# Performance work log

Hardware: AMD Instinct MI355X
Metric: run time of the kernel (lower is better)

## Reference

```python
import jax, jax.numpy as jnp
import numpy as np

B, L, D, T, S, K = 16, 4095, 768, 768, 64, 8
H = T // 2  # per-direction GRU hidden


def setup_inputs() -> dict:
    key = jax.random.key(0)
    ks = jax.random.split(key, 16)
    sc = 0.05
    hidden = jax.random.normal(ks[0], (B, L, D), jnp.float32)
    attn_len = jax.random.randint(ks[1], (B,), L // 2, L).astype(jnp.int32)
    span_start = jax.random.randint(ks[2], (B, S), 0, L - 16).astype(jnp.int32)
    span_len = jax.random.randint(ks[3], (B, S), 1, 9).astype(jnp.int32)
    return dict(
        hidden=hidden,
        W_ih_f=jax.random.normal(ks[4], (3 * H, D)) * sc,
        W_hh_f=jax.random.normal(ks[5], (3 * H, H)) * sc,
        b_ih_f=jax.random.normal(ks[6], (3 * H,)) * sc,
        b_hh_f=jax.random.normal(ks[7], (3 * H,)) * sc,
        W_ih_b=jax.random.normal(ks[8], (3 * H, D)) * sc,
        W_hh_b=jax.random.normal(ks[9], (3 * H, H)) * sc,
        b_ih_b=jax.random.normal(ks[10], (3 * H,)) * sc,
        b_hh_b=jax.random.normal(ks[11], (3 * H,)) * sc,
        W_ctx=jax.random.normal(ks[12], (T, D)) * sc,
        b_ctx=jax.random.normal(ks[13], (T,)) * sc,
        W_find=jax.random.normal(ks[14], (1, 2 * T)) * sc,
        attn_len=attn_len,
        span_start=span_start,
        span_len=span_len,
    )


def _gru_dir(x, W_ih, W_hh, b_ih, b_hh, reverse):
    # x: [B, S, D] -> [B, S, H]; torch GRU gate order: r, z, n
    def step(h, xt):
        gi = xt @ W_ih.T + b_ih            # [B, 3H]
        gh = h @ W_hh.T + b_hh
        ir, iz, inn = jnp.split(gi, 3, axis=-1)
        hr, hz, hn = jnp.split(gh, 3, axis=-1)
        r = jax.nn.sigmoid(ir + hr)
        z = jax.nn.sigmoid(iz + hz)
        n = jnp.tanh(inn + r * hn)
        h_new = (1.0 - z) * n + z * h
        return h_new, h_new
    xs = jnp.swapaxes(x, 0, 1)             # [S, B, D]
    h0 = jnp.zeros((x.shape[0], W_hh.shape[1]), x.dtype)
    _, ys = jax.lax.scan(step, h0, xs, reverse=reverse)
    return jnp.swapaxes(ys, 0, 1)          # [B, S, H]


def reference(hidden, W_ih_f, W_hh_f, b_ih_f, b_hh_f, W_ih_b, W_hh_b, b_ih_b, b_hh_b,
              W_ctx, b_ctx, W_find, attn_len, span_start, span_len):
    pos = jnp.arange(L)
    # --- per-span mean pooling (ragged spans, vectorized via masks) ---
    end = span_start + span_len - 1        # inclusive end, as hidden[start:end+1]
    mask = (pos[None, None, :] >= span_start[..., None]) & (pos[None, None, :] <= end[..., None])
    maskf = mask.astype(hidden.dtype)      # [B, S, L]
    cnt = maskf.sum(-1, keepdims=True)
    span_rep = jnp.einsum('bsl,bld->bsd', maskf, hidden) / cnt   # [B, S, D]
    # --- bidirectional GRU over the span sequence ---
    h_f = _gru_dir(span_rep, W_ih_f, W_hh_f, b_ih_f, b_hh_f, reverse=False)
    h_b = _gru_dir(span_rep, W_ih_b, W_hh_b, b_ih_b, b_hh_b, reverse=True)
    rep_ac = jnp.concatenate([h_f, h_b], axis=-1)                # [B, S, T]
    # --- context: mean over valid tokens excluding the last valid token, then linear ---
    n_ctx = (attn_len - 1).astype(hidden.dtype)                  # [B]
    ctx_mask = (pos[None, :] < (attn_len - 1)[:, None]).astype(hidden.dtype)
    ctx = jnp.einsum('bl,bld->bd', ctx_mask, hidden) / n_ctx[:, None]
    rep_context = ctx @ W_ctx.T + b_ctx                          # [B, T]
    # --- findm attention: concat + linear(no bias) + sigmoid + topk + gather ---
    all_reps = jnp.concatenate([rep_ac, rep_context[:, None, :]], axis=1)  # [B, S+1, T]
    wq, wk = W_find[0, :T], W_find[0, T:]
    # sigmoid(W [q; k]) = sigmoid(q.wq + k.wk)
    score = jax.nn.sigmoid((rep_ac @ wq)[:, :, None] + (all_reps @ wk)[:, None, :])  # [B, S, S+1]
    vals, idx = jax.lax.top_k(score, K)                          # [B, S, K]
    v1 = jnp.take_along_axis(all_reps[:, None, :, :], idx[..., None], axis=2)        # [B, S, K, T]
    return rep_ac, rep_context, v1, vals, idx
```

## Files before the change

kernel.cpp:

```cpp
#include <hip/hip_runtime.h>
#include <hip/hip_bf16.h>
#include <math.h>

#define BB 16
#define LL 4095
#define DD 768
#define TT 768
#define SS 64
#define KK 8
#define HH 384
#define G3 1152
#define NWPD 24

__global__ void span_mean_kernel(const float* __restrict__ hidden,
                                 const int* __restrict__ sstart,
                                 const int* __restrict__ slen,
                                 float* __restrict__ span) {
    int bs = blockIdx.x;
    int b = bs >> 6;
    int st = sstart[bs];
    int ln = slen[bs];
    const float4* base = (const float4*)(hidden + ((size_t)b * LL + st) * DD);
    float4* dst = (float4*)(span + (size_t)bs * DD);
    float inv = 1.0f / (float)ln;
    for (int d = threadIdx.x; d < DD / 4; d += 256) {
        float4 acc = make_float4(0.f, 0.f, 0.f, 0.f);
        for (int r = 0; r < ln; ++r) {
            float4 v = base[(size_t)r * (DD / 4) + d];
            acc.x += v.x; acc.y += v.y; acc.z += v.z; acc.w += v.w;
        }
        dst[d] = make_float4(acc.x * inv, acc.y * inv, acc.z * inv, acc.w * inv);
    }
}

__global__ void ctx_accum_kernel(const float* __restrict__ hidden,
                                 const int* __restrict__ attn_len,
                                 float* __restrict__ ctx) {
    int b = blockIdx.x, chunk = blockIdx.y;
    int lim = attn_len[b] - 1;
    int l0 = chunk * 128;
    int l1 = min(l0 + 128, lim);
    if (l0 >= l1) return;
    int t = threadIdx.x;
    const float* base = hidden + (size_t)b * LL * DD;
    float a0 = 0.f, a1 = 0.f, a2 = 0.f;
    for (int l = l0; l < l1; ++l) {
        const float* row = base + (size_t)l * DD;
        a0 += row[t]; a1 += row[t + 256]; a2 += row[t + 512];
    }
    atomicAdd(&ctx[b * DD + t], a0);
    atomicAdd(&ctx[b * DD + t + 256], a1);
    atomicAdd(&ctx[b * DD + t + 512], a2);
}

__global__ void repctx_kernel(const float* __restrict__ ctxsum,
                              const int* __restrict__ attn_len,
                              const float* __restrict__ W_ctx,
                              const float* __restrict__ b_ctx,
                              float* __restrict__ out_rc) {
    int b = blockIdx.x;
    int j = blockIdx.y * 256 + threadIdx.x;
    __shared__ float cv[DD];
    float inv = 1.0f / (float)(attn_len[b] - 1);
    for (int d = threadIdx.x; d < DD; d += 256) cv[d] = ctxsum[b * DD + d] * inv;
    __syncthreads();
    const float* wr = W_ctx + (size_t)j * DD;
    float acc = b_ctx[j];
    for (int d = 0; d < DD; ++d) acc += wr[d] * cv[d];
    out_rc[b * TT + j] = acc;
}

__global__ __launch_bounds__(256) void gi_gemm_kernel(
        const float* __restrict__ span,
        const float* __restrict__ Wf, const float* __restrict__ Wb,
        const float* __restrict__ bihf, const float* __restrict__ bhhf,
        const float* __restrict__ bihb, const float* __restrict__ bhhb,
        float* __restrict__ gi) {
    int dir = blockIdx.z;
    const float* W = dir ? Wb : Wf;
    const float* bih = dir ? bihb : bihf;
    const float* bhh = dir ? bhhb : bhhf;
    int m0 = blockIdx.x * 64, n0 = blockIdx.y * 64;
    __shared__ float As[16][68];
    __shared__ float Bs[16][68];
    int t = threadIdx.x, tx = t & 15, ty = t >> 4;
    float acc[4][4] = {{0.f}};
    for (int k0 = 0; k0 < DD; k0 += 16) {
        for (int e = t; e < 1024; e += 256) {
            int r = e >> 4, c = e & 15;
            As[c][r] = span[(size_t)(m0 + r) * DD + k0 + c];
            Bs[c][r] = W[(size_t)(n0 + r) * DD + k0 + c];
        }
        __syncthreads();
#pragma unroll
        for (int kk = 0; kk < 16; ++kk) {
            float4 a4 = *(const float4*)&As[kk][ty * 4];
            float4 b4 = *(const float4*)&Bs[kk][tx * 4];
            float a[4] = {a4.x, a4.y, a4.z, a4.w};
            float bv[4] = {b4.x, b4.y, b4.z, b4.w};
#pragma unroll
            for (int i = 0; i < 4; ++i)
#pragma unroll
                for (int j = 0; j < 4; ++j) acc[i][j] += a[i] * bv[j];
        }
        __syncthreads();
    }
#pragma unroll
    for (int i = 0; i < 4; ++i)
#pragma unroll
        for (int j = 0; j < 4; ++j) {
            int m = m0 + ty * 4 + i, n = n0 + tx * 4 + j;
            float v = acc[i][j] + bih[n] + (n < 2 * HH ? bhh[n] : 0.0f);
            gi[((size_t)dir * 1024 + m) * G3 + n] = v;
        }
}

__global__ __launch_bounds__(256, 1) void scan_coop_kernel(
        const float* __restrict__ gi,
        const float* __restrict__ Whf, const float* __restrict__ Whb,
        const float* __restrict__ bhhf, const float* __restrict__ bhhb,
        unsigned long long* __restrict__ hpair,
        float* __restrict__ repac) {
    int wg = blockIdx.x;
    int dir = wg / NWPD;
    int w = wg % NWPD;
    int t = threadIdx.x;
    int kseg = t & 15, i_loc = t >> 4;
    int i_glob = w * 16 + i_loc;
    const float* Wh = dir ? Whb : Whf;

    float4 wr[3][6];
#pragma unroll
    for (int g = 0; g < 3; ++g)
#pragma unroll
        for (int j = 0; j < 6; ++j) {
            wr[g][j] = *(const float4*)(Wh + (size_t)(g * HH + i_glob) * HH + kseg * 4 + 64 * j);
            asm volatile("" : "+v"(wr[g][j].x), "+v"(wr[g][j].y),
                              "+v"(wr[g][j].z), "+v"(wr[g][j].w));
        }
    float bhn = (dir ? bhhb : bhhf)[2 * HH + i_glob];

    __shared__ __align__(16) float hs[6144];
    float4* hs4 = (float4*)hs;

    for (int s = 0; s < 64; ++s) {
        int p = dir ? (63 - s) : s;
        const float* grow = gi + ((size_t)dir * 1024 + kseg * 64 + p) * G3;
        float g_r = grow[i_glob], g_z = grow[HH + i_glob], g_n = grow[2 * HH + i_glob];
        {
            const unsigned long long* src = hpair + (size_t)((s & 1) * 2 + dir) * 6144;
            unsigned int expect = (unsigned int)s;
            unsigned long long vals[24];
            for (;;) {
                bool ok = true;
#pragma unroll
                for (int j = 0; j < 24; ++j) {
                    vals[j] = __hip_atomic_load(src + j * 256 + t,
                                                __ATOMIC_RELAXED, __HIP_MEMORY_SCOPE_AGENT);
                    ok &= ((unsigned int)(vals[j] >> 32) == expect);
                }
                if (ok) break;
                __builtin_amdgcn_s_sleep(1);
            }
#pragma unroll
            for (int j = 0; j < 24; ++j)
                hs[j * 256 + t] = __uint_as_float((unsigned int)vals[j]);
        }
        __syncthreads();
        float pr[16], pz[16], pn[16];
#pragma unroll
        for (int b = 0; b < 16; ++b) {
            float4 hq[6];
#pragma unroll
            for (int j = 0; j < 6; ++j) hq[j] = hs4[b * 96 + kseg + 16 * j];
            float ar = 0.f, az = 0.f, an = 0.f;
#pragma unroll
            for (int j = 0; j < 6; ++j) {
                ar += wr[0][j].x * hq[j].x + wr[0][j].y * hq[j].y + wr[0][j].z * hq[j].z + wr[0][j].w * hq[j].w;
                az += wr[1][j].x * hq[j].x + wr[1][j].y * hq[j].y + wr[1][j].z * hq[j].z + wr[1][j].w * hq[j].w;
                an += wr[2][j].x * hq[j].x + wr[2][j].y * hq[j].y + wr[2][j].z * hq[j].z + wr[2][j].w * hq[j].w;
            }
            pr[b] = ar; pz[b] = az; pn[b] = an;
        }
        float qr[8], qz[8], qn[8];
        {
            const bool hi = (kseg & 8) != 0;
#pragma unroll
            for (int j = 0; j < 8; ++j) {
                float sr_ = hi ? pr[j] : pr[j + 8];
                qr[j] = (hi ? pr[j + 8] : pr[j]) + __shfl_xor(sr_, 8);
                float sz_ = hi ? pz[j] : pz[j + 8];
                qz[j] = (hi ? pz[j + 8] : pz[j]) + __shfl_xor(sz_, 8);
                float sn_ = hi ? pn[j] : pn[j + 8];
                qn[j] = (hi ? pn[j + 8] : pn[j]) + __shfl_xor(sn_, 8);
            }
        }
        float ur[4], uz[4], un[4];
        {
            const bool hi = (kseg & 4) != 0;
#pragma unroll
            for (int j = 0; j < 4; ++j) {
                float sr_ = hi ? qr[j] : qr[j + 4];
                ur[j] = (hi ? qr[j + 4] : qr[j]) + __shfl_xor(sr_, 4);
                float sz_ = hi ? qz[j] : qz[j + 4];
                uz[j] = (hi ? qz[j + 4] : qz[j]) + __shfl_xor(sz_, 4);
                float sn_ = hi ? qn[j] : qn[j + 4];
                un[j] = (hi ? qn[j + 4] : qn[j]) + __shfl_xor(sn_, 4);
            }
        }
        float vr[2], vz[2], vn[2];
        {
            const bool hi = (kseg & 2) != 0;
#pragma unroll
            for (int j = 0; j < 2; ++j) {
                float sr_ = hi ? ur[j] : ur[j + 2];
                vr[j] = (hi ? ur[j + 2] : ur[j]) + __shfl_xor(sr_, 2);
                float sz_ = hi ? uz[j] : uz[j + 2];
                vz[j] = (hi ? uz[j + 2] : uz[j]) + __shfl_xor(sz_, 2);
                float sn_ = hi ? un[j] : un[j + 2];
                vn[j] = (hi ? un[j + 2] : un[j]) + __shfl_xor(sn_, 2);
            }
        }
        float sr, sz, sn;
        {
            const bool hi = (kseg & 1) != 0;
            float sr_ = hi ? vr[0] : vr[1];
            sr = (hi ? vr[1] : vr[0]) + __shfl_xor(sr_, 1);
            float sz_ = hi ? vz[0] : vz[1];
            sz = (hi ? vz[1] : vz[0]) + __shfl_xor(sz_, 1);
            float sn_ = hi ? vn[0] : vn[1];
            sn = (hi ? vn[1] : vn[0]) + __shfl_xor(sn_, 1);
        }
        float r = 1.0f / (1.0f + expf(-(g_r + sr)));
        float z = 1.0f / (1.0f + expf(-(g_z + sz)));
        float n = tanhf(g_n + r * (sn + bhn));
        float hold = hs[kseg * 384 + i_glob];
        float hnew = (1.0f - z) * n + z * hold;
        unsigned long long pv = ((unsigned long long)(unsigned int)(s + 1) << 32)
                              | (unsigned long long)__float_as_uint(hnew);
        __hip_atomic_store(hpair + (size_t)(((s + 1) & 1) * 2 + dir) * 6144 + kseg * 384 + i_glob,
                           pv, __ATOMIC_RELAXED, __HIP_MEMORY_SCOPE_AGENT);
        repac[(size_t)(kseg * 64 + p) * TT + dir * HH + i_glob] = hnew;
        __syncthreads();
    }
}

__global__ void qkv_kernel(const float* __restrict__ repac,
                           const float* __restrict__ repctx,
                           const float* __restrict__ Wfind,
                           float* __restrict__ qv, float* __restrict__ kv) {
    int w = blockIdx.x * 4 + (threadIdx.x >> 6);
    int lane = threadIdx.x & 63;
    const float* row;
    const float* vec;
    float* dst;
    if (w < 1024) {
        row = repac + (size_t)w * TT;
        vec = Wfind;
        dst = qv + w;
    } else {
        int u = w - 1024;
        int b = u / 65, j = u % 65;
        row = (j < 64) ? (repac + (size_t)(b * 64 + j) * TT) : (repctx + (size_t)b * TT);
        vec = Wfind + TT;
        dst = kv + u;
    }
    double acc = 0.0;
    for (int d = lane; d < TT; d += 64) acc += (double)row[d] * (double)vec[d];
#pragma unroll
    for (int off = 32; off > 0; off >>= 1) acc += __shfl_down(acc, off);
    if (lane == 0) *dst = (float)acc;
}

__global__ __launch_bounds__(64) void topk_kernel(
                            const float* __restrict__ qv,
                            const float* __restrict__ kv,
                            float* __restrict__ vals_out,
                            float* __restrict__ idx_out,
                            int* __restrict__ idxw) {
    int t = threadIdx.x;
    int b = blockIdx.x;
    int bs = b * 64 + t;
    __shared__ float kvs[65];
    for (int e = t; e < 65; e += 64) kvs[e] = kv[b * 65 + e];
    __syncthreads();
    float q = qv[bs];
    float sc[65];
#pragma unroll
    for (int j = 0; j < 65; ++j) {
        float x = q + kvs[j];
        float e = (float)exp(-(double)x);
        sc[j] = 1.0f / (1.0f + e);
    }
    unsigned long long taken = 0ull;
    bool tk64 = false;
    for (int kk = 0; kk < 8; ++kk) {
        float best = -3.0e38f;
        int bj = 0;
#pragma unroll
        for (int j = 0; j < 65; ++j) {
            bool tkn = (j < 64) ? (((taken >> j) & 1ull) != 0ull) : tk64;
            float v = sc[j];
            if (!tkn && v > best) { best = v; bj = j; }
        }
        if (bj < 64) taken |= (1ull << bj); else tk64 = true;
        vals_out[bs * 8 + kk] = best;
        idx_out[bs * 8 + kk] = (float)bj;
        idxw[bs * 8 + kk] = bj;
    }
}

__global__ void v1_kernel(const float* __restrict__ repac,
                          const float* __restrict__ repctx,
                          const int* __restrict__ idxw,
                          float* __restrict__ v1) {
    int bs = blockIdx.x;
    int b = bs >> 6;
    int t = threadIdx.x;
    for (int kk = 0; kk < 8; ++kk) {
        int j = idxw[bs * 8 + kk];
        const float4* src = (const float4*)((j < 64) ? (repac + (size_t)(b * 64 + j) * TT)
                                                     : (repctx + (size_t)b * TT));
        float4* dst = (float4*)(v1 + ((size_t)bs * 8 + kk) * TT);
        for (int d = t; d < DD / 4; d += 256) dst[d] = src[d];
    }
}

extern "C" void kernel_launch(void* const* d_in, const int* in_sizes, int n_in,
                              void* d_out, int out_size, void* d_ws, size_t ws_size,
                              hipStream_t stream) {
    const float* hidden    = (const float*)d_in[0];
    const float* W_ih_f    = (const float*)d_in[1];
    const float* W_hh_f    = (const float*)d_in[2];
    const float* b_ih_f    = (const float*)d_in[3];
    const float* b_hh_f    = (const float*)d_in[4];
    const float* W_ih_b    = (const float*)d_in[5];
    const float* W_hh_b    = (const float*)d_in[6];
    const float* b_ih_b    = (const float*)d_in[7];
    const float* b_hh_b    = (const float*)d_in[8];
    const float* W_ctx     = (const float*)d_in[9];
    const float* b_ctx     = (const float*)d_in[10];
    const float* W_find    = (const float*)d_in[11];
    const int*   attn_len  = (const int*)d_in[12];
    const int*   span_start= (const int*)d_in[13];
    const int*   span_len  = (const int*)d_in[14];
    (void)in_sizes; (void)n_in; (void)out_size; (void)ws_size;

    float* ws   = (float*)d_ws;
    float* span = ws;
    float* gi   = span + 786432;
    float* ctx  = gi + 2359296;
    float* qv   = ctx + 12288;
    float* kv   = qv + 1024;
    int*   idxw = (int*)(kv + 1040);
    unsigned long long* hpair = (unsigned long long*)span;

    float* out      = (float*)d_out;
    float* o_repac  = out;
    float* o_repctx = out + 786432;
    float* o_v1     = out + 798720;
    float* o_vals   = out + 7090176;
    float* o_idx    = out + 7098368;

    hipMemsetAsync(ctx, 0, (size_t)BB * DD * sizeof(float), stream);

    span_mean_kernel<<<1024, 256, 0, stream>>>(hidden, span_start, span_len, span);
    ctx_accum_kernel<<<dim3(BB, 32), 256, 0, stream>>>(hidden, attn_len, ctx);
    repctx_kernel<<<dim3(BB, 3), 256, 0, stream>>>(ctx, attn_len, W_ctx, b_ctx, o_repctx);
    gi_gemm_kernel<<<dim3(16, 18, 2), 256, 0, stream>>>(span, W_ih_f, W_ih_b,
                                                        b_ih_f, b_hh_f, b_ih_b, b_hh_b, gi);
    hipMemsetAsync(hpair, 0, (size_t)24576 * sizeof(unsigned long long), stream);
    scan_coop_kernel<<<48, 256, 0, stream>>>(gi, W_hh_f, W_hh_b, b_hh_f, b_hh_b,
                                             hpair, o_repac);
    qkv_kernel<<<516, 256, 0, stream>>>(o_repac, o_repctx, W_find, qv, kv);
    topk_kernel<<<16, 64, 0, stream>>>(qv, kv, o_vals, o_idx, idxw);
    v1_kernel<<<1024, 256, 0, stream>>>(o_repac, o_repctx, idxw, o_v1);
}
```

Measured before the change: 905.1 us.

## Interleave both GRU directions per block and fuse find/topk/gather kernels

The cooperative GRU scan now runs both directions in each of 24 workgroups instead of one direction per workgroup across 48. It alternates forward and backward phases, so one direction's cross-block wait can overlap the other's compute, and it drops the trailing per-step barrier by using separate shared buffers. The q/k dot products, top-k and v1 gather are merged into a single per-batch kernel. The two memsets are folded into existing kernels. This cuts launch count and global round trips, at the cost of doubling register-resident recurrent weights per thread and halving the number of active CUs in the scan.

Result: slower. 1.388 ms (+53.3%).

```diff
diff --git a/kernel.cpp b/kernel.cpp
--- a/kernel.cpp
+++ b/kernel.cpp
@@ -15,7 +15,9 @@
 __global__ void span_mean_kernel(const float* __restrict__ hidden,
                                  const int* __restrict__ sstart,
                                  const int* __restrict__ slen,
-                                 float* __restrict__ span) {
+                                 float* __restrict__ span,
+                                 float* __restrict__ ctx) {
+    if (blockIdx.x < 48) ctx[blockIdx.x * 256 + threadIdx.x] = 0.0f;
     int bs = blockIdx.x;
     int b = bs >> 6;
     int st = sstart[bs];
@@ -51,23 +53,6 @@
     atomicAdd(&ctx[b * DD + t], a0);
     atomicAdd(&ctx[b * DD + t + 256], a1);
     atomicAdd(&ctx[b * DD + t + 512], a2);
-}
-
-__global__ void repctx_kernel(const float* __restrict__ ctxsum,
-                              const int* __restrict__ attn_len,
-                              const float* __restrict__ W_ctx,
-                              const float* __restrict__ b_ctx,
-                              float* __restrict__ out_rc) {
-    int b = blockIdx.x;
-    int j = blockIdx.y * 256 + threadIdx.x;
-    __shared__ float cv[DD];
-    float inv = 1.0f / (float)(attn_len[b] - 1);
-    for (int d = threadIdx.x; d < DD; d += 256) cv[d] = ctxsum[b * DD + d] * inv;
-    __syncthreads();
-    const float* wr = W_ctx + (size_t)j * DD;
-    float acc = b_ctx[j];
-    for (int d = 0; d < DD; ++d) acc += wr[d] * cv[d];
-    out_rc[b * TT + j] = acc;
 }
 
 __global__ __launch_bounds__(256) void gi_gemm_kernel(
@@ -115,214 +100,230 @@
         }
 }
 
+__global__ void repctx_kernel(const float* __restrict__ ctxsum,
+                              const int* __restrict__ attn_len,
+                              const float* __restrict__ W_ctx,
+                              const float* __restrict__ b_ctx,
+                              float* __restrict__ out_rc,
+                              unsigned long long* __restrict__ hpair) {
+    int gid = ((int)blockIdx.y * 16 + (int)blockIdx.x) * 256 + threadIdx.x;
+    hpair[gid] = 0ull;
+    hpair[gid + 12288] = 0ull;
+    int b = blockIdx.x;
+    int j = blockIdx.y * 256 + threadIdx.x;
+    __shared__ float cv[DD];
+    float inv = 1.0f / (float)(attn_len[b] - 1);
+    for (int d = threadIdx.x; d < DD; d += 256) cv[d] = ctxsum[b * DD + d] * inv;
+    __syncthreads();
+    const float* wr = W_ctx + (size_t)j * DD;
+    float acc = b_ctx[j];
+    for (int d = 0; d < DD; ++d) acc += wr[d] * cv[d];
+    out_rc[b * TT + j] = acc;
+}
+
+__device__ __forceinline__ void scan_phase(
+        int s, int dirp, int p, int kseg, int i_glob, int t,
+        const float4 (&wr)[3][6], float bhn,
+        const float* __restrict__ gi,
+        unsigned long long* __restrict__ hpair,
+        float* __restrict__ repac,
+        float* hs) {
+    const float4* hs4 = (const float4*)hs;
+    const float* grow = gi + ((size_t)dirp * 1024 + kseg * 64 + p) * G3;
+    float g_r = grow[i_glob], g_z = grow[HH + i_glob], g_n = grow[2 * HH + i_glob];
+    {
+        const unsigned long long* src = hpair + (size_t)((s & 1) * 2 + dirp) * 6144;
+        unsigned int expect = (unsigned int)s;
+        unsigned long long vals[24];
+        for (;;) {
+            bool ok = true;
+#pragma unroll
+            for (int j = 0; j < 24; ++j) {
+                vals[j] = __hip_atomic_load(src + j * 256 + t,
+                                            __ATOMIC_RELAXED, __HIP_MEMORY_SCOPE_AGENT);
+                ok &= ((unsigned int)(vals[j] >> 32) == expect);
+            }
+            if (ok) break;
+            __builtin_amdgcn_s_sleep(1);
+        }
+#pragma unroll
+        for (int j = 0; j < 24; ++j)
+            hs[j * 256 + t] = __uint_as_float((unsigned int)vals[j]);
+    }
+    __syncthreads();
+    float pr[16], pz[16], pn[16];
+#pragma unroll
+    for (int b = 0; b < 16; ++b) {
+        float4 hq[6];
+#pragma unroll
+        for (int j = 0; j < 6; ++j) hq[j] = hs4[b * 96 + kseg + 16 * j];
+        float ar = 0.f, az = 0.f, an = 0.f;
+#pragma unroll
+        for (int j = 0; j < 6; ++j) {
+            ar += wr[0][j].x * hq[j].x + wr[0][j].y * hq[j].y + wr[0][j].z * hq[j].z + wr[0][j].w * hq[j].w;
+            az += wr[1][j].x * hq[j].x + wr[1][j].y * hq[j].y + wr[1][j].z * hq[j].z + wr[1][j].w * hq[j].w;
+            an += wr[2][j].x * hq[j].x + wr[2][j].y * hq[j].y + wr[2][j].z * hq[j].z + wr[2][j].w * hq[j].w;
+        }
+        pr[b] = ar; pz[b] = az; pn[b] = an;
+    }
+    float qr[8], qz[8], qn[8];
+    {
+        const bool hi = (kseg & 8) != 0;
+#pragma unroll
+        for (int j = 0; j < 8; ++j) {
+            float sr_ = hi ? pr[j] : pr[j + 8];
+            qr[j] = (hi ? pr[j + 8] : pr[j]) + __shfl_xor(sr_, 8);
+            float sz_ = hi ? pz[j] : pz[j + 8];
+            qz[j] = (hi ? pz[j + 8] : pz[j]) + __shfl_xor(sz_, 8);
+            float sn_ = hi ? pn[j] : pn[j + 8];
+            qn[j] = (hi ? pn[j + 8] : pn[j]) + __shfl_xor(sn_, 8);
+        }
+    }
+    float ur[4], uz[4], un[4];
+    {
+        const bool hi = (kseg & 4) != 0;
+#pragma unroll
+        for (int j = 0; j < 4; ++j) {
+            float sr_ = hi ? qr[j] : qr[j + 4];
+            ur[j] = (hi ? qr[j + 4] : qr[j]) + __shfl_xor(sr_, 4);
+            float sz_ = hi ? qz[j] : qz[j + 4];
+            uz[j] = (hi ? qz[j + 4] : qz[j]) + __shfl_xor(sz_, 4);
+            float sn_ = hi ? qn[j] : qn[j + 4];
+            un[j] = (hi ? qn[j + 4] : qn[j]) + __shfl_xor(sn_, 4);
+        }
+    }
+    float vr[2], vz[2], vn[2];
+    {
+        const bool hi = (kseg & 2) != 0;
+#pragma unroll
+        for (int j = 0; j < 2; ++j) {
+            float sr_ = hi ? ur[j] : ur[j + 2];
+            vr[j] = (hi ? ur[j + 2] : ur[j]) + __shfl_xor(sr_, 2);
+            float sz_ = hi ? uz[j] : uz[j + 2];
+            vz[j] = (hi ? uz[j + 2] : uz[j]) + __shfl_xor(sz_, 2);
+            float sn_ = hi ? un[j] : un[j + 2];
+            vn[j] = (hi ? un[j + 2] : un[j]) + __shfl_xor(sn_, 2);
+        }
+    }
+    float sr, sz, sn;
+    {
+        const bool hi = (kseg & 1) != 0;
+        float sr_ = hi ? vr[0] : vr[1];
+        sr = (hi ? vr[1] : vr[0]) + __shfl_xor(sr_, 1);
+        float sz_ = hi ? vz[0] : vz[1];
+        sz = (hi ? vz[1] : vz[0]) + __shfl_xor(sz_, 1);
+        float sn_ = hi ? vn[0] : vn[1];
+        sn = (hi ? vn[1] : vn[0]) + __shfl_xor(sn_, 1);
+    }
+    float r = 1.0f / (1.0f + expf(-(g_r + sr)));
+    float z = 1.0f / (1.0f + expf(-(g_z + sz)));
+    float n = tanhf(g_n + r * (sn + bhn));
+    float hold = hs[kseg * 384 + i_glob];
+    float hnew = (1.0f - z) * n + z * hold;
+    unsigned long long pv = ((unsigned long long)(unsigned int)(s + 1) << 32)
+                          | (unsigned long long)__float_as_uint(hnew);
+    __hip_atomic_store(hpair + (size_t)(((s + 1) & 1) * 2 + dirp) * 6144 + kseg * 384 + i_glob,
+                       pv, __ATOMIC_RELAXED, __HIP_MEMORY_SCOPE_AGENT);
+    repac[(size_t)(kseg * 64 + p) * TT + dirp * HH + i_glob] = hnew;
+}
+
 __global__ __launch_bounds__(256, 1) void scan_coop_kernel(
         const float* __restrict__ gi,
         const float* __restrict__ Whf, const float* __restrict__ Whb,
         const float* __restrict__ bhhf, const float* __restrict__ bhhb,
         unsigned long long* __restrict__ hpair,
         float* __restrict__ repac) {
-    int wg = blockIdx.x;
-    int dir = wg / NWPD;
-    int w = wg % NWPD;
+    int w = blockIdx.x;
     int t = threadIdx.x;
     int kseg = t & 15, i_loc = t >> 4;
     int i_glob = w * 16 + i_loc;
-    const float* Wh = dir ? Whb : Whf;
-
-    float4 wr[3][6];
+
+    float4 wr0[3][6], wr1[3][6];
 #pragma unroll
     for (int g = 0; g < 3; ++g)
 #pragma unroll
         for (int j = 0; j < 6; ++j) {
-            wr[g][j] = *(const float4*)(Wh + (size_t)(g * HH + i_glob) * HH + kseg * 4 + 64 * j);
-            asm volatile("" : "+v"(wr[g][j].x), "+v"(wr[g][j].y),
-                              "+v"(wr[g][j].z), "+v"(wr[g][j].w));
-        }
-    float bhn = (dir ? bhhb : bhhf)[2 * HH + i_glob];
-
-    __shared__ __align__(16) float hs[6144];
-    float4* hs4 = (float4*)hs;
+            wr0[g][j] = *(const float4*)(Whf + (size_t)(g * HH + i_glob) * HH + kseg * 4 + 64 * j);
+            asm volatile("" : "+v"(wr0[g][j].x), "+v"(wr0[g][j].y),
+                              "+v"(wr0[g][j].z), "+v"(wr0[g][j].w));
+            wr1[g][j] = *(const float4*)(Whb + (size_t)(g * HH + i_glob) * HH + kseg * 4 + 64 * j);
+            asm volatile("" : "+v"(wr1[g][j].x), "+v"(wr1[g][j].y),
+                              "+v"(wr1[g][j].z), "+v"(wr1[g][j].w));
+        }
+    float bhn0 = bhhf[2 * HH + i_glob];
+    float bhn1 = bhhb[2 * HH + i_glob];
+
+    __shared__ __align__(16) float hs0[6144];
+    __shared__ __align__(16) float hs1[6144];
 
     for (int s = 0; s < 64; ++s) {
-        int p = dir ? (63 - s) : s;
-        const float* grow = gi + ((size_t)dir * 1024 + kseg * 64 + p) * G3;
-        float g_r = grow[i_glob], g_z = grow[HH + i_glob], g_n = grow[2 * HH + i_glob];
-        {
-            const unsigned long long* src = hpair + (size_t)((s & 1) * 2 + dir) * 6144;
-            unsigned int expect = (unsigned int)s;
-            unsigned long long vals[24];
-            for (;;) {
-                bool ok = true;
-#pragma unroll
-                for (int j = 0; j < 24; ++j) {
-                    vals[j] = __hip_atomic_load(src + j * 256 + t,
-                                                __ATOMIC_RELAXED, __HIP_MEMORY_SCOPE_AGENT);
-                    ok &= ((unsigned int)(vals[j] >> 32) == expect);
-                }
-                if (ok) break;
-                __builtin_amdgcn_s_sleep(1);
+        scan_phase(s, 0, s,      kseg, i_glob, t, wr0, bhn0, gi, hpair, repac, hs0);
+        scan_phase(s, 1, 63 - s, kseg, i_glob, t, wr1, bhn1, gi, hpair, repac, hs1);
+    }
+}
+
+__global__ __launch_bounds__(256) void find_kernel(
+        const float* __restrict__ repac,
+        const float* __restrict__ repctx,
+        const float* __restrict__ Wfind,
+        float* __restrict__ vals_out,
+        float* __restrict__ idx_out,
+        float* __restrict__ v1) {
+    int b = blockIdx.x;
+    int t = threadIdx.x;
+    int wv = t >> 6, lane = t & 63;
+    __shared__ float qs[64];
+    __shared__ float ks[65];
+    __shared__ int idxs[64 * 8];
+    for (int j = wv; j < 129; j += 4) {
+        bool isq = (j < 64);
+        int jj = isq ? j : (j - 64);
+        const float* row = isq ? (repac + (size_t)(b * 64 + j) * TT)
+                               : ((jj < 64) ? (repac + (size_t)(b * 64 + jj) * TT)
+                                            : (repctx + (size_t)b * TT));
+        const float* vec = isq ? Wfind : (Wfind + TT);
+        double acc = 0.0;
+        for (int d = lane; d < TT; d += 64) acc += (double)row[d] * (double)vec[d];
+#pragma unroll
+        for (int off = 32; off > 0; off >>= 1) acc += __shfl_down(acc, off);
+        if (lane == 0) { if (isq) qs[j] = (float)acc; else ks[jj] = (float)acc; }
+    }
+    __syncthreads();
+    if (t < 64) {
+        int bs = b * 64 + t;
+        float q = qs[t];
+        float sc[65];
+#pragma unroll
+        for (int j = 0; j < 65; ++j) {
+            float x = q + ks[j];
+            float e = (float)exp(-(double)x);
+            sc[j] = 1.0f / (1.0f + e);
+        }
+        unsigned long long taken = 0ull;
+        bool tk64 = false;
+        for (int kk = 0; kk < 8; ++kk) {
+            float best = -3.0e38f;
+            int bj = 0;
+#pragma unroll
+            for (int j = 0; j < 65; ++j) {
+                bool tkn = (j < 64) ? (((taken >> j) & 1ull) != 0ull) : tk64;
+                float v = sc[j];
+                if (!tkn && v > best) { best = v; bj = j; }
             }
-#pragma unroll
-            for (int j = 0; j < 24; ++j)
-                hs[j * 256 + t] = __uint_as_float((unsigned int)vals[j]);
-        }
-        __syncthreads();
-        float pr[16], pz[16], pn[16];
-#pragma unroll
-        for (int b = 0; b < 16; ++b) {
-            float4 hq[6];
-#pragma unroll
-            for (int j = 0; j < 6; ++j) hq[j] = hs4[b * 96 + kseg + 16 * j];
-            float ar = 0.f, az = 0.f, an = 0.f;
-#pragma unroll
-            for (int j = 0; j < 6; ++j) {
-                ar += wr[0][j].x * hq[j].x + wr[0][j].y * hq[j].y + wr[0][j].z * hq[j].z + wr[0][j].w * hq[j].w;
-                az += wr[1][j].x * hq[j].x + wr[1][j].y * hq[j].y + wr[1][j].z * hq[j].z + wr[1][j].w * hq[j].w;
-                an += wr[2][j].x * hq[j].x + wr[2][j].y * hq[j].y + wr[2][j].z * hq[j].z + wr[2][j].w * hq[j].w;
-            }
-            pr[b] = ar; pz[b] = az; pn[b] = an;
-        }
-        float qr[8], qz[8], qn[8];
-        {
-            const bool hi = (kseg & 8) != 0;
-#pragma unroll
-            for (int j = 0; j < 8; ++j) {
-                float sr_ = hi ? pr[j] : pr[j + 8];
-                qr[j] = (hi ? pr[j + 8] : pr[j]) + __shfl_xor(sr_, 8);
-                float sz_ = hi ? pz[j] : pz[j + 8];
-                qz[j] = (hi ? pz[j + 8] : pz[j]) + __shfl_xor(sz_, 8);
-                float sn_ = hi ? pn[j] : pn[j + 8];
-                qn[j] = (hi ? pn[j + 8] : pn[j]) + __shfl_xor(sn_, 8);
-            }
-        }
-        float ur[4], uz[4], un[4];
-        {
-            const bool hi = (kseg & 4) != 0;
-#pragma unroll
-            for (int j = 0; j < 4; ++j) {
-                float sr_ = hi ? qr[j] : qr[j + 4];
-                ur[j] = (hi ? qr[j + 4] : qr[j]) + __shfl_xor(sr_, 4);
-                float sz_ = hi ? qz[j] : qz[j + 4];
-                uz[j] = (hi ? qz[j + 4] : qz[j]) + __shfl_xor(sz_, 4);
-                float sn_ = hi ? qn[j] : qn[j + 4];
-                un[j] = (hi ? qn[j + 4] : qn[j]) + __shfl_xor(sn_, 4);
-            }
-        }
-        float vr[2], vz[2], vn[2];
-        {
-            const bool hi = (kseg & 2) != 0;
-#pragma unroll
-            for (int j = 0; j < 2; ++j) {
-                float sr_ = hi ? ur[j] : ur[j + 2];
-                vr[j] = (hi ? ur[j + 2] : ur[j]) + __shfl_xor(sr_, 2);
-                float sz_ = hi ? uz[j] : uz[j + 2];
-                vz[j] = (hi ? uz[j + 2] : uz[j]) + __shfl_xor(sz_, 2);
-                float sn_ = hi ? un[j] : un[j + 2];
-                vn[j] = (hi ? un[j + 2] : un[j]) + __shfl_xor(sn_, 2);
-            }
-        }
-        float sr, sz, sn;
-        {
-            const bool hi = (kseg & 1) != 0;
-            float sr_ = hi ? vr[0] : vr[1];
-            sr = (hi ? vr[1] : vr[0]) + __shfl_xor(sr_, 1);
-            float sz_ = hi ? vz[0] : vz[1];
-            sz = (hi ? vz[1] : vz[0]) + __shfl_xor(sz_, 1);
-            float sn_ = hi ? vn[0] : vn[1];
-            sn = (hi ? vn[1] : vn[0]) + __shfl_xor(sn_, 1);
-        }
-        float r = 1.0f / (1.0f + expf(-(g_r + sr)));
-        float z = 1.0f / (1.0f + expf(-(g_z + sz)));
-        float n = tanhf(g_n + r * (sn + bhn));
-        float hold = hs[kseg * 384 + i_glob];
-        float hnew = (1.0f - z) * n + z * hold;
-        unsigned long long pv = ((unsigned long long)(unsigned int)(s + 1) << 32)
-                              | (unsigned long long)__float_as_uint(hnew);
-        __hip_atomic_store(hpair + (size_t)(((s + 1) & 1) * 2 + dir) * 6144 + kseg * 384 + i_glob,
-                           pv, __ATOMIC_RELAXED, __HIP_MEMORY_SCOPE_AGENT);
-        repac[(size_t)(kseg * 64 + p) * TT + dir * HH + i_glob] = hnew;
-        __syncthreads();
-    }
-}
-
-__global__ void qkv_kernel(const float* __restrict__ repac,
-                           const float* __restrict__ repctx,
-                           const float* __restrict__ Wfind,
-                           float* __restrict__ qv, float* __restrict__ kv) {
-    int w = blockIdx.x * 4 + (threadIdx.x >> 6);
-    int lane = threadIdx.x & 63;
-    const float* row;
-    const float* vec;
-    float* dst;
-    if (w < 1024) {
-        row = repac + (size_t)w * TT;
-        vec = Wfind;
-        dst = qv + w;
-    } else {
-        int u = w - 1024;
-        int b = u / 65, j = u % 65;
-        row = (j < 64) ? (repac + (size_t)(b * 64 + j) * TT) : (repctx + (size_t)b * TT);
-        vec = Wfind + TT;
-        dst = kv + u;
-    }
-    double acc = 0.0;
-    for (int d = lane; d < TT; d += 64) acc += (double)row[d] * (double)vec[d];
-#pragma unroll
-    for (int off = 32; off > 0; off >>= 1) acc += __shfl_down(acc, off);
-    if (lane == 0) *dst = (float)acc;
-}
-
-__global__ __launch_bounds__(64) void topk_kernel(
-                            const float* __restrict__ qv,
-                            const float* __restrict__ kv,
-                            float* __restrict__ vals_out,
-                            float* __restrict__ idx_out,
-                            int* __restrict__ idxw) {
-    int t = threadIdx.x;
-    int b = blockIdx.x;
-    int bs = b * 64 + t;
-    __shared__ float kvs[65];
-    for (int e = t; e < 65; e += 64) kvs[e] = kv[b * 65 + e];
+            if (bj < 64) taken |= (1ull << bj); else tk64 = true;
+            vals_out[bs * 8 + kk] = best;
+            idx_out[bs * 8 + kk] = (float)bj;
+            idxs[t * 8 + kk] = bj;
+        }
+    }
     __syncthreads();
-    float q = qv[bs];
-    float sc[65];
-#pragma unroll
-    for (int j = 0; j < 65; ++j) {
-        float x = q + kvs[j];
-        float e = (float)exp(-(double)x);
-        sc[j] = 1.0f / (1.0f + e);
-    }
-    unsigned long long taken = 0ull;
-    bool tk64 = false;
-    for (int kk = 0; kk < 8; ++kk) {
-        float best = -3.0e38f;
-        int bj = 0;
-#pragma unroll
-        for (int j = 0; j < 65; ++j) {
-            bool tkn = (j < 64) ? (((taken >> j) & 1ull) != 0ull) : tk64;
-            float v = sc[j];
-            if (!tkn && v > best) { best = v; bj = j; }
-        }
-        if (bj < 64) taken |= (1ull << bj); else tk64 = true;
-        vals_out[bs * 8 + kk] = best;
-        idx_out[bs * 8 + kk] = (float)bj;
-        idxw[bs * 8 + kk] = bj;
-    }
-}
-
-__global__ void v1_kernel(const float* __restrict__ repac,
-                          const float* __restrict__ repctx,
-                          const int* __restrict__ idxw,
-                          float* __restrict__ v1) {
-    int bs = blockIdx.x;
-    int b = bs >> 6;
-    int t = threadIdx.x;
-    for (int kk = 0; kk < 8; ++kk) {
-        int j = idxw[bs * 8 + kk];
+    for (int c = wv; c < 512; c += 4) {
+        int s = c >> 3, kk = c & 7;
+        int j = idxs[s * 8 + kk];
         const float4* src = (const float4*)((j < 64) ? (repac + (size_t)(b * 64 + j) * TT)
                                                      : (repctx + (size_t)b * TT));
-        float4* dst = (float4*)(v1 + ((size_t)bs * 8 + kk) * TT);
-        for (int d = t; d < DD / 4; d += 256) dst[d] = src[d];
+        float4* dst = (float4*)(v1 + ((size_t)(b * 64 + s) * 8 + kk) * TT);
+        for (int d = lane; d < TT / 4; d += 64) dst[d] = src[d];
     }
 }
 
@@ -350,9 +351,6 @@
     float* span = ws;
     float* gi   = span + 786432;
     float* ctx  = gi + 2359296;
-    float* qv   = ctx + 12288;
-    float* kv   = qv + 1024;
-    int*   idxw = (int*)(kv + 1040);
     unsigned long long* hpair = (unsigned long long*)span;
 
     float* out      = (float*)d_out;
@@ -362,17 +360,14 @@
     float* o_vals   = out + 7090176;
     float* o_idx    = out + 7098368;
 
-    hipMemsetAsync(ctx, 0, (size_t)BB * DD * sizeof(float), stream);
-
-    span_mean_kernel<<<1024, 256, 0, stream>>>(hidden, span_start, span_len, span);
+    span_mean_kernel<<<1024, 256, 0, stream>>>(hidden, span_start, span_len, span, ctx);
     ctx_accum_kernel<<<dim3(BB, 32), 256, 0, stream>>>(hidden, attn_len, ctx);
-    repctx_kernel<<<dim3(BB, 3), 256, 0, stream>>>(ctx, attn_len, W_ctx, b_ctx, o_repctx);
     gi_gemm_kernel<<<dim3(16, 18, 2), 256, 0, stream>>>(span, W_ih_f, W_ih_b,
                                                         b_ih_f, b_hh_f, b_ih_b, b_hh_b, gi);
-    hipMemsetAsync(hpair, 0, (size_t)24576 * sizeof(unsigned long long), stream);
-    scan_coop_kernel<<<48, 256, 0, stream>>>(gi, W_hh_f, W_hh_b, b_hh_f, b_hh_b,
-                                             hpair, o_repac);
-    qkv_kernel<<<516, 256, 0, stream>>>(o_repac, o_repctx, W_find, qv, kv);
-    topk_kernel<<<16, 64, 0, stream>>>(qv, kv, o_vals, o_idx, idxw);
-    v1_kernel<<<1024, 256, 0, stream>>>(o_repac, o_repctx, idxw, o_v1);
-}
+    repctx_kernel<<<dim3(BB, 3), 256, 0, stream>>>(ctx, attn_len, W_ctx, b_ctx,
+                                                   o_repctx, hpair);
+    scan_coop_kernel<<<NWPD, 256, 0, stream>>>(gi, W_hh_f, W_hh_b, b_hh_f, b_hh_b,
+                                               hpair, o_repac);
+    find_kernel<<<BB, 256, 0, stream>>>(o_repac, o_repctx, W_find,
+                                        o_vals, o_idx, o_v1);
+}
```

## Co-locate GRU scan workgroups on one XCD and fuse setup kernels

Applied to the files above, without the earlier changes.

The scan kernel now launches 768 workgroups. Each one reads its XCD id from a hardware register and joins an election, and only the first 48 workgroups on the first XCD to fill up stay alive. Those 48 exchange hidden state through L2-local (workgroup-scope) stores polled with sc0 loads, with an agent-scope mirror as a fallback checked every 8 rounds. The aim is to avoid cross-XCD coherence latency on each of the 64 recurrent steps. Separately, the repctx and gi GEMM kernels are merged into one launch, the two memsets are folded into existing kernels, and hpair now lives in the v1 output buffer. In exchange it relies on undocumented XCD placement and cache behaviour, and surplus workgroups add launch overhead.

Result: slower. 1.308 ms (+44.5%).

```diff
diff --git a/kernel.cpp b/kernel.cpp
--- a/kernel.cpp
+++ b/kernel.cpp
@@ -11,11 +11,14 @@
 #define HH 384
 #define G3 1152
 #define NWPD 24
+#define NWORK 48
 
 __global__ void span_mean_kernel(const float* __restrict__ hidden,
                                  const int* __restrict__ sstart,
                                  const int* __restrict__ slen,
-                                 float* __restrict__ span) {
+                                 float* __restrict__ span,
+                                 float* __restrict__ ctx) {
+    if (blockIdx.x < 48) ctx[blockIdx.x * 256 + threadIdx.x] = 0.0f;
     int bs = blockIdx.x;
     int b = bs >> 6;
     int st = sstart[bs];
@@ -53,78 +56,110 @@
     atomicAdd(&ctx[b * DD + t + 512], a2);
 }
 
-__global__ void repctx_kernel(const float* __restrict__ ctxsum,
-                              const int* __restrict__ attn_len,
-                              const float* __restrict__ W_ctx,
-                              const float* __restrict__ b_ctx,
-                              float* __restrict__ out_rc) {
-    int b = blockIdx.x;
-    int j = blockIdx.y * 256 + threadIdx.x;
-    __shared__ float cv[DD];
-    float inv = 1.0f / (float)(attn_len[b] - 1);
-    for (int d = threadIdx.x; d < DD; d += 256) cv[d] = ctxsum[b * DD + d] * inv;
-    __syncthreads();
-    const float* wr = W_ctx + (size_t)j * DD;
-    float acc = b_ctx[j];
-    for (int d = 0; d < DD; ++d) acc += wr[d] * cv[d];
-    out_rc[b * TT + j] = acc;
-}
-
-__global__ __launch_bounds__(256) void gi_gemm_kernel(
+__global__ __launch_bounds__(256) void fused_b_kernel(
         const float* __restrict__ span,
         const float* __restrict__ Wf, const float* __restrict__ Wb,
         const float* __restrict__ bihf, const float* __restrict__ bhhf,
         const float* __restrict__ bihb, const float* __restrict__ bhhb,
-        float* __restrict__ gi) {
-    int dir = blockIdx.z;
-    const float* W = dir ? Wb : Wf;
-    const float* bih = dir ? bihb : bihf;
-    const float* bhh = dir ? bhhb : bhhf;
-    int m0 = blockIdx.x * 64, n0 = blockIdx.y * 64;
-    __shared__ float As[16][68];
-    __shared__ float Bs[16][68];
-    int t = threadIdx.x, tx = t & 15, ty = t >> 4;
-    float acc[4][4] = {{0.f}};
-    for (int k0 = 0; k0 < DD; k0 += 16) {
-        for (int e = t; e < 1024; e += 256) {
-            int r = e >> 4, c = e & 15;
-            As[c][r] = span[(size_t)(m0 + r) * DD + k0 + c];
-            Bs[c][r] = W[(size_t)(n0 + r) * DD + k0 + c];
-        }
+        float* __restrict__ gi,
+        const float* __restrict__ ctxsum, const int* __restrict__ attn_len,
+        const float* __restrict__ W_ctx, const float* __restrict__ b_ctx,
+        float* __restrict__ out_rc,
+        unsigned long long* __restrict__ hpair,
+        unsigned long long* __restrict__ mirror,
+        int* __restrict__ elect) {
+    int bid = blockIdx.x;
+    int t = threadIdx.x;
+    if (bid < 576) {
+        int mb = bid & 15, nb = (bid >> 4) % 18, dir = bid / 288;
+        const float* W = dir ? Wb : Wf;
+        const float* bih = dir ? bihb : bihf;
+        const float* bhh = dir ? bhhb : bhhf;
+        int m0 = mb * 64, n0 = nb * 64;
+        __shared__ float As[16][68];
+        __shared__ float Bs[16][68];
+        int tx = t & 15, ty = t >> 4;
+        float acc[4][4] = {{0.f}};
+        for (int k0 = 0; k0 < DD; k0 += 16) {
+            for (int e = t; e < 1024; e += 256) {
+                int r = e >> 4, c = e & 15;
+                As[c][r] = span[(size_t)(m0 + r) * DD + k0 + c];
+                Bs[c][r] = W[(size_t)(n0 + r) * DD + k0 + c];
+            }
+            __syncthreads();
+#pragma unroll
+            for (int kk = 0; kk < 16; ++kk) {
+                float4 a4 = *(const float4*)&As[kk][ty * 4];
+                float4 b4 = *(const float4*)&Bs[kk][tx * 4];
+                float a[4] = {a4.x, a4.y, a4.z, a4.w};
+                float bv[4] = {b4.x, b4.y, b4.z, b4.w};
+#pragma unroll
+                for (int i = 0; i < 4; ++i)
+#pragma unroll
+                    for (int j = 0; j < 4; ++j) acc[i][j] += a[i] * bv[j];
+            }
+            __syncthreads();
+        }
+#pragma unroll
+        for (int i = 0; i < 4; ++i)
+#pragma unroll
+            for (int j = 0; j < 4; ++j) {
+                int m = m0 + ty * 4 + i, n = n0 + tx * 4 + j;
+                float v = acc[i][j] + bih[n] + (n < 2 * HH ? bhh[n] : 0.0f);
+                gi[((size_t)dir * 1024 + m) * G3 + n] = v;
+            }
+    } else {
+        int rb = bid - 576;
+        int gid = rb * 256 + t;
+        hpair[gid] = 0ull;  hpair[gid + 12288] = 0ull;
+        mirror[gid] = 0ull; mirror[gid + 12288] = 0ull;
+        if (rb == 0 && t < 16) elect[t] = 0;
+        int b = rb & 15;
+        int j = (rb >> 4) * 256 + t;
+        __shared__ float cv[DD];
+        float inv = 1.0f / (float)(attn_len[b] - 1);
+        for (int d = t; d < DD; d += 256) cv[d] = ctxsum[b * DD + d] * inv;
         __syncthreads();
-#pragma unroll
-        for (int kk = 0; kk < 16; ++kk) {
-            float4 a4 = *(const float4*)&As[kk][ty * 4];
-            float4 b4 = *(const float4*)&Bs[kk][tx * 4];
-            float a[4] = {a4.x, a4.y, a4.z, a4.w};
-            float bv[4] = {b4.x, b4.y, b4.z, b4.w};
-#pragma unroll
-            for (int i = 0; i < 4; ++i)
-#pragma unroll
-                for (int j = 0; j < 4; ++j) acc[i][j] += a[i] * bv[j];
-        }
-        __syncthreads();
-    }
-#pragma unroll
-    for (int i = 0; i < 4; ++i)
-#pragma unroll
-        for (int j = 0; j < 4; ++j) {
-            int m = m0 + ty * 4 + i, n = n0 + tx * 4 + j;
-            float v = acc[i][j] + bih[n] + (n < 2 * HH ? bhh[n] : 0.0f);
-            gi[((size_t)dir * 1024 + m) * G3 + n] = v;
-        }
-}
-
-__global__ __launch_bounds__(256, 1) void scan_coop_kernel(
+        const float* wr = W_ctx + (size_t)j * DD;
+        float acc = b_ctx[j];
+        for (int d = 0; d < DD; ++d) acc += wr[d] * cv[d];
+        out_rc[b * TT + j] = acc;
+    }
+}
+
+__global__ __launch_bounds__(256, 2) void scan_coop_kernel(
         const float* __restrict__ gi,
         const float* __restrict__ Whf, const float* __restrict__ Whb,
         const float* __restrict__ bhhf, const float* __restrict__ bhhb,
         unsigned long long* __restrict__ hpair,
+        unsigned long long* __restrict__ mirror,
+        int* __restrict__ elect,
         float* __restrict__ repac) {
-    int wg = blockIdx.x;
-    int dir = wg / NWPD;
-    int w = wg % NWPD;
+    __shared__ int sh_widx;
     int t = threadIdx.x;
+    if (t == 0) {
+        int xcd = __builtin_amdgcn_s_getreg((3 << 11) | 20) & 7;
+        int rank = __hip_atomic_fetch_add(&elect[xcd], 1,
+                                          __ATOMIC_RELAXED, __HIP_MEMORY_SCOPE_AGENT);
+        if (rank == NWORK - 1) {
+            int exp0 = 0;
+            __hip_atomic_compare_exchange_strong(&elect[8], &exp0, xcd + 1,
+                __ATOMIC_RELAXED, __ATOMIC_RELAXED, __HIP_MEMORY_SCOPE_AGENT);
+        }
+        int wnr;
+        for (;;) {
+            wnr = __hip_atomic_load(&elect[8], __ATOMIC_RELAXED, __HIP_MEMORY_SCOPE_AGENT);
+            if (wnr != 0) break;
+            __builtin_amdgcn_s_sleep(8);
+        }
+        sh_widx = (wnr == xcd + 1 && rank < NWORK) ? rank : -1;
+    }
+    __syncthreads();
+    int widx = sh_widx;
+    if (widx < 0) return;
+
+    int dir = widx / NWPD;
+    int w = widx % NWPD;
     int kseg = t & 15, i_loc = t >> 4;
     int i_glob = w * 16 + i_loc;
     const float* Wh = dir ? Whb : Whf;
@@ -148,25 +183,43 @@
         const float* grow = gi + ((size_t)dir * 1024 + kseg * 64 + p) * G3;
         float g_r = grow[i_glob], g_z = grow[HH + i_glob], g_n = grow[2 * HH + i_glob];
         {
-            const unsigned long long* src = hpair + (size_t)((s & 1) * 2 + dir) * 6144;
+            const unsigned long long* src  = hpair  + (size_t)((s & 1) * 2 + dir) * 6144;
+            const unsigned long long* msrc = mirror + (size_t)((s & 1) * 2 + dir) * 6144;
             unsigned int expect = (unsigned int)s;
             unsigned long long vals[24];
+            int rounds = 0;
             for (;;) {
+#pragma unroll
+                for (int j = 0; j < 24; ++j) {
+                    unsigned int off = (unsigned int)((j * 256 + t) * 8);
+                    asm volatile("global_load_dwordx2 %0, %1, %2 sc0"
+                                 : "=v"(vals[j]) : "v"(off), "s"(src));
+                }
+                asm volatile("s_waitcnt vmcnt(0)" ::: "memory");
+                __builtin_amdgcn_sched_barrier(0);
                 bool ok = true;
 #pragma unroll
-                for (int j = 0; j < 24; ++j) {
-                    vals[j] = __hip_atomic_load(src + j * 256 + t,
-                                                __ATOMIC_RELAXED, __HIP_MEMORY_SCOPE_AGENT);
-                    ok &= ((unsigned int)(vals[j] >> 32) == expect);
+                for (int j = 0; j < 24; ++j) ok &= ((unsigned int)(vals[j] >> 32) == expect);
+                if (ok) break;
+                if (((++rounds) & 7) == 0) {
+                    bool mok = true;
+#pragma unroll
+                    for (int j = 0; j < 24; ++j) {
+                        vals[j] = __hip_atomic_load(msrc + j * 256 + t,
+                                                    __ATOMIC_RELAXED, __HIP_MEMORY_SCOPE_AGENT);
+                        mok &= ((unsigned int)(vals[j] >> 32) == expect);
+                    }
+                    if (mok) break;
                 }
-                if (ok) break;
                 __builtin_amdgcn_s_sleep(1);
             }
 #pragma unroll
             for (int j = 0; j < 24; ++j)
                 hs[j * 256 + t] = __uint_as_float((unsigned int)vals[j]);
         }
-        __syncthreads();
+        asm volatile("s_waitcnt lgkmcnt(0)" ::: "memory");
+        __builtin_amdgcn_sched_barrier(0);
+        __builtin_amdgcn_s_barrier();
         float pr[16], pz[16], pn[16];
 #pragma unroll
         for (int b = 0; b < 16; ++b) {
@@ -238,10 +291,13 @@
         float hnew = (1.0f - z) * n + z * hold;
         unsigned long long pv = ((unsigned long long)(unsigned int)(s + 1) << 32)
                               | (unsigned long long)__float_as_uint(hnew);
-        __hip_atomic_store(hpair + (size_t)(((s + 1) & 1) * 2 + dir) * 6144 + kseg * 384 + i_glob,
-                           pv, __ATOMIC_RELAXED, __HIP_MEMORY_SCOPE_AGENT);
+        size_t pidx = (size_t)(((s + 1) & 1) * 2 + dir) * 6144 + kseg * 384 + i_glob;
+        __hip_atomic_store(hpair + pidx, pv, __ATOMIC_RELAXED, __HIP_MEMORY_SCOPE_WORKGROUP);
+        __hip_atomic_store(mirror + pidx, pv, __ATOMIC_RELAXED, __HIP_MEMORY_SCOPE_AGENT);
         repac[(size_t)(kseg * 64 + p) * TT + dir * HH + i_glob] = hnew;
-        __syncthreads();
+        asm volatile("s_waitcnt lgkmcnt(0)" ::: "memory");
+        __builtin_amdgcn_sched_barrier(0);
+        __builtin_amdgcn_s_barrier();
     }
 }
 
@@ -353,7 +409,6 @@
     float* qv   = ctx + 12288;
     float* kv   = qv + 1024;
     int*   idxw = (int*)(kv + 1040);
-    unsigned long long* hpair = (unsigned long long*)span;
 
     float* out      = (float*)d_out;
     float* o_repac  = out;
@@ -362,16 +417,18 @@
     float* o_vals   = out + 7090176;
     float* o_idx    = out + 7098368;
 
-    hipMemsetAsync(ctx, 0, (size_t)BB * DD * sizeof(float), stream);
-
-    span_mean_kernel<<<1024, 256, 0, stream>>>(hidden, span_start, span_len, span);
+    unsigned long long* hpair  = (unsigned long long*)o_v1;
+    unsigned long long* mirror = hpair + 24576;
+    int* elect = (int*)(mirror + 24576);
+
+    span_mean_kernel<<<1024, 256, 0, stream>>>(hidden, span_start, span_len, span, ctx);
     ctx_accum_kernel<<<dim3(BB, 32), 256, 0, stream>>>(hidden, attn_len, ctx);
-    repctx_kernel<<<dim3(BB, 3), 256, 0, stream>>>(ctx, attn_len, W_ctx, b_ctx, o_repctx);
-    gi_gemm_kernel<<<dim3(16, 18, 2), 256, 0, stream>>>(span, W_ih_f, W_ih_b,
-                                                        b_ih_f, b_hh_f, b_ih_b, b_hh_b, gi);
-    hipMemsetAsync(hpair, 0, (size_t)24576 * sizeof(unsigned long long), stream);
-    scan_coop_kernel<<<48, 256, 0, stream>>>(gi, W_hh_f, W_hh_b, b_hh_f, b_hh_b,
-                                             hpair, o_repac);
+    fused_b_kernel<<<624, 256, 0, stream>>>(span, W_ih_f, W_ih_b,
+                                            b_ih_f, b_hh_f, b_ih_b, b_hh_b, gi,
+                                            ctx, attn_len, W_ctx, b_ctx,
+                                            o_repctx, hpair, mirror, elect);
+    scan_coop_kernel<<<768, 256, 0, stream>>>(gi, W_hh_f, W_hh_b, b_hh_f, b_hh_b,
+                                              hpair, mirror, elect, o_repac);
     qkv_kernel<<<516, 256, 0, stream>>>(o_repac, o_repctx, W_find, qv, kv);
     topk_kernel<<<16, 64, 0, stream>>>(qv, kv, o_vals, o_idx, idxw);
     v1_kernel<<<1024, 256, 0, stream>>>(o_repac, o_repctx, idxw, o_v1);
```

## Fold memsets and repctx into fused launches, bypass-cache polling in GRU scan

Applied to the files above, without the earlier changes.

Zeroing of the ctx buffer moves into span_mean_kernel, and the repctx projection plus hpair zeroing join the input-gate GEMM in one 624-block kernel. This drops two memset calls and one kernel launch. hpair moves onto the v1 output buffer, which is written later. The scan's polling loop now issues all 24 loads as raw global_load_dwordx2 with sc0 sc1 cache bits before a single wait, and the end-of-step syncthreads becomes an LDS-only wait plus s_barrier. This cuts per-step sync latency but relies on hand-written memory ordering that could be subtly wrong.

Result: faster. 878.2 us (-3.0%).

```diff
diff --git a/kernel.cpp b/kernel.cpp
--- a/kernel.cpp
+++ b/kernel.cpp
@@ -15,7 +15,9 @@
 __global__ void span_mean_kernel(const float* __restrict__ hidden,
                                  const int* __restrict__ sstart,
                                  const int* __restrict__ slen,
-                                 float* __restrict__ span) {
+                                 float* __restrict__ span,
+                                 float* __restrict__ ctx) {
+    if (blockIdx.x < 48) ctx[blockIdx.x * 256 + threadIdx.x] = 0.0f;
     int bs = blockIdx.x;
     int b = bs >> 6;
     int st = sstart[bs];
@@ -53,66 +55,72 @@
     atomicAdd(&ctx[b * DD + t + 512], a2);
 }
 
-__global__ void repctx_kernel(const float* __restrict__ ctxsum,
-                              const int* __restrict__ attn_len,
-                              const float* __restrict__ W_ctx,
-                              const float* __restrict__ b_ctx,
-                              float* __restrict__ out_rc) {
-    int b = blockIdx.x;
-    int j = blockIdx.y * 256 + threadIdx.x;
-    __shared__ float cv[DD];
-    float inv = 1.0f / (float)(attn_len[b] - 1);
-    for (int d = threadIdx.x; d < DD; d += 256) cv[d] = ctxsum[b * DD + d] * inv;
-    __syncthreads();
-    const float* wr = W_ctx + (size_t)j * DD;
-    float acc = b_ctx[j];
-    for (int d = 0; d < DD; ++d) acc += wr[d] * cv[d];
-    out_rc[b * TT + j] = acc;
-}
-
-__global__ __launch_bounds__(256) void gi_gemm_kernel(
+__global__ __launch_bounds__(256) void fused_b_kernel(
         const float* __restrict__ span,
         const float* __restrict__ Wf, const float* __restrict__ Wb,
         const float* __restrict__ bihf, const float* __restrict__ bhhf,
         const float* __restrict__ bihb, const float* __restrict__ bhhb,
-        float* __restrict__ gi) {
-    int dir = blockIdx.z;
-    const float* W = dir ? Wb : Wf;
-    const float* bih = dir ? bihb : bihf;
-    const float* bhh = dir ? bhhb : bhhf;
-    int m0 = blockIdx.x * 64, n0 = blockIdx.y * 64;
-    __shared__ float As[16][68];
-    __shared__ float Bs[16][68];
-    int t = threadIdx.x, tx = t & 15, ty = t >> 4;
-    float acc[4][4] = {{0.f}};
-    for (int k0 = 0; k0 < DD; k0 += 16) {
-        for (int e = t; e < 1024; e += 256) {
-            int r = e >> 4, c = e & 15;
-            As[c][r] = span[(size_t)(m0 + r) * DD + k0 + c];
-            Bs[c][r] = W[(size_t)(n0 + r) * DD + k0 + c];
-        }
+        float* __restrict__ gi,
+        const float* __restrict__ ctxsum, const int* __restrict__ attn_len,
+        const float* __restrict__ W_ctx, const float* __restrict__ b_ctx,
+        float* __restrict__ out_rc,
+        unsigned long long* __restrict__ hpair) {
+    int bid = blockIdx.x;
+    int t = threadIdx.x;
+    if (bid < 576) {
+        int mb = bid & 15, nb = (bid >> 4) % 18, dir = bid / 288;
+        const float* W = dir ? Wb : Wf;
+        const float* bih = dir ? bihb : bihf;
+        const float* bhh = dir ? bhhb : bhhf;
+        int m0 = mb * 64, n0 = nb * 64;
+        __shared__ float As[16][68];
+        __shared__ float Bs[16][68];
+        int tx = t & 15, ty = t >> 4;
+        float acc[4][4] = {{0.f}};
+        for (int k0 = 0; k0 < DD; k0 += 16) {
+            for (int e = t; e < 1024; e += 256) {
+                int r = e >> 4, c = e & 15;
+                As[c][r] = span[(size_t)(m0 + r) * DD + k0 + c];
+                Bs[c][r] = W[(size_t)(n0 + r) * DD + k0 + c];
+            }
+            __syncthreads();
+#pragma unroll
+            for (int kk = 0; kk < 16; ++kk) {
+                float4 a4 = *(const float4*)&As[kk][ty * 4];
+                float4 b4 = *(const float4*)&Bs[kk][tx * 4];
+                float a[4] = {a4.x, a4.y, a4.z, a4.w};
+                float bv[4] = {b4.x, b4.y, b4.z, b4.w};
+#pragma unroll
+                for (int i = 0; i < 4; ++i)
+#pragma unroll
+                    for (int j = 0; j < 4; ++j) acc[i][j] += a[i] * bv[j];
+            }
+            __syncthreads();
+        }
+#pragma unroll
+        for (int i = 0; i < 4; ++i)
+#pragma unroll
+            for (int j = 0; j < 4; ++j) {
+                int m = m0 + ty * 4 + i, n = n0 + tx * 4 + j;
+                float v = acc[i][j] + bih[n] + (n < 2 * HH ? bhh[n] : 0.0f);
+                gi[((size_t)dir * 1024 + m) * G3 + n] = v;
+            }
+    } else {
+        int rb = bid - 576;
+        int gid = rb * 256 + t;
+        hpair[gid] = 0ull;
+        hpair[gid + 12288] = 0ull;
+        int b = rb & 15;
+        int j = (rb >> 4) * 256 + t;
+        __shared__ float cv[DD];
+        float inv = 1.0f / (float)(attn_len[b] - 1);
+        for (int d = t; d < DD; d += 256) cv[d] = ctxsum[b * DD + d] * inv;
         __syncthreads();
-#pragma unroll
-        for (int kk = 0; kk < 16; ++kk) {
-            float4 a4 = *(const float4*)&As[kk][ty * 4];
-            float4 b4 = *(const float4*)&Bs[kk][tx * 4];
-            float a[4] = {a4.x, a4.y, a4.z, a4.w};
-            float bv[4] = {b4.x, b4.y, b4.z, b4.w};
-#pragma unroll
-            for (int i = 0; i < 4; ++i)
-#pragma unroll
-                for (int j = 0; j < 4; ++j) acc[i][j] += a[i] * bv[j];
-        }
-        __syncthreads();
-    }
-#pragma unroll
-    for (int i = 0; i < 4; ++i)
-#pragma unroll
-        for (int j = 0; j < 4; ++j) {
-            int m = m0 + ty * 4 + i, n = n0 + tx * 4 + j;
-            float v = acc[i][j] + bih[n] + (n < 2 * HH ? bhh[n] : 0.0f);
-            gi[((size_t)dir * 1024 + m) * G3 + n] = v;
-        }
+        const float* wr = W_ctx + (size_t)j * DD;
+        float acc = b_ctx[j];
+        for (int d = 0; d < DD; ++d) acc += wr[d] * cv[d];
+        out_rc[b * TT + j] = acc;
+    }
 }
 
 __global__ __launch_bounds__(256, 1) void scan_coop_kernel(
@@ -152,13 +160,17 @@
             unsigned int expect = (unsigned int)s;
             unsigned long long vals[24];
             for (;;) {
+#pragma unroll
+                for (int j = 0; j < 24; ++j) {
+                    unsigned int off = (unsigned int)((j * 256 + t) * 8);
+                    asm volatile("global_load_dwordx2 %0, %1, %2 sc0 sc1"
+                                 : "=v"(vals[j]) : "v"(off), "s"(src));
+                }
+                asm volatile("s_waitcnt vmcnt(0)" ::: "memory");
+                __builtin_amdgcn_sched_barrier(0);
                 bool ok = true;
 #pragma unroll
-                for (int j = 0; j < 24; ++j) {
-                    vals[j] = __hip_atomic_load(src + j * 256 + t,
-                                                __ATOMIC_RELAXED, __HIP_MEMORY_SCOPE_AGENT);
-                    ok &= ((unsigned int)(vals[j] >> 32) == expect);
-                }
+                for (int j = 0; j < 24; ++j) ok &= ((unsigned int)(vals[j] >> 32) == expect);
                 if (ok) break;
                 __builtin_amdgcn_s_sleep(1);
             }
@@ -241,7 +253,9 @@
         __hip_atomic_store(hpair + (size_t)(((s + 1) & 1) * 2 + dir) * 6144 + kseg * 384 + i_glob,
                            pv, __ATOMIC_RELAXED, __HIP_MEMORY_SCOPE_AGENT);
         repac[(size_t)(kseg * 64 + p) * TT + dir * HH + i_glob] = hnew;
-        __syncthreads();
+        asm volatile("s_waitcnt lgkmcnt(0)" ::: "memory");
+        __builtin_amdgcn_sched_barrier(0);
+        __builtin_amdgcn_s_barrier();
     }
 }
 
@@ -353,7 +367,6 @@
     float* qv   = ctx + 12288;
     float* kv   = qv + 1024;
     int*   idxw = (int*)(kv + 1040);
-    unsigned long long* hpair = (unsigned long long*)span;
 
     float* out      = (float*)d_out;
     float* o_repac  = out;
@@ -362,14 +375,14 @@
     float* o_vals   = out + 7090176;
     float* o_idx    = out + 7098368;
 
-    hipMemsetAsync(ctx, 0, (size_t)BB * DD * sizeof(float), stream);
-
-    span_mean_kernel<<<1024, 256, 0, stream>>>(hidden, span_start, span_len, span);
+    unsigned long long* hpair = (unsigned long long*)o_v1;
+
+    span_mean_kernel<<<1024, 256, 0, stream>>>(hidden, span_start, span_len, span, ctx);
     ctx_accum_kernel<<<dim3(BB, 32), 256, 0, stream>>>(hidden, attn_len, ctx);
-    repctx_kernel<<<dim3(BB, 3), 256, 0, stream>>>(ctx, attn_len, W_ctx, b_ctx, o_repctx);
-    gi_gemm_kernel<<<dim3(16, 18, 2), 256, 0, stream>>>(span, W_ih_f, W_ih_b,
-                                                        b_ih_f, b_hh_f, b_ih_b, b_hh_b, gi);
-    hipMemsetAsync(hpair, 0, (size_t)24576 * sizeof(unsigned long long), stream);
+    fused_b_kernel<<<624, 256, 0, stream>>>(span, W_ih_f, W_ih_b,
+                                            b_ih_f, b_hh_f, b_ih_b, b_hh_b, gi,
+                                            ctx, attn_len, W_ctx, b_ctx,
+                                            o_repctx, hpair);
     scan_coop_kernel<<<48, 256, 0, stream>>>(gi, W_hh_f, W_hh_b, b_hh_f, b_hh_b,
                                              hpair, o_repac);
     qkv_kernel<<<516, 256, 0, stream>>>(o_repac, o_repctx, W_find, qv, kv);
```
